# Optimization experiments

Measured on AMD Instinct MI355X. Metric: run time of the kernel, lower is better.

## Reference

```python
import jax, jax.numpy as jnp
import numpy as np

D_MODEL = 512
N_HEADS = 8
EDGE_FEAT_DIM = 4
NUM_GRAPHS = 64
NODES_PER_GRAPH = 128
N_NODES = NUM_GRAPHS * NODES_PER_GRAPH          # 8192
EDGES_PER_GRAPH = 4096                           # avg degree 32
N_EDGES = NUM_GRAPHS * EDGES_PER_GRAPH           # 262144


def setup_inputs() -> dict:
    key = jax.random.key(0)
    ks = jax.random.split(key, 12)
    s = 0.02
    x = jax.random.normal(ks[0], (N_NODES, D_MODEL), jnp.float32)
    # edges constrained within their graph (block-diagonal structure)
    g_of_e = jnp.arange(N_EDGES, dtype=jnp.int32) // EDGES_PER_GRAPH
    src = g_of_e * NODES_PER_GRAPH + jax.random.randint(ks[1], (N_EDGES,), 0, NODES_PER_GRAPH, jnp.int32)
    dst = g_of_e * NODES_PER_GRAPH + jax.random.randint(ks[2], (N_EDGES,), 0, NODES_PER_GRAPH, jnp.int32)
    edge_index = jnp.stack([src, dst]).astype(jnp.int32)
    edge_attr = jax.random.normal(ks[3], (N_EDGES, EDGE_FEAT_DIM), jnp.float32)
    batch = jnp.repeat(jnp.arange(NUM_GRAPHS, dtype=jnp.int32), NODES_PER_GRAPH)
    # projection weights (in,out) convention: y = x @ W + b
    Wq = jax.random.normal(ks[4], (D_MODEL, D_MODEL), jnp.float32) * s
    Wk = jax.random.normal(ks[5], (D_MODEL, D_MODEL), jnp.float32) * s
    Wv = jax.random.normal(ks[6], (D_MODEL, D_MODEL), jnp.float32) * s
    Wo = jax.random.normal(ks[7], (D_MODEL, D_MODEL), jnp.float32) * s
    bq = jnp.zeros((D_MODEL,), jnp.float32)
    bk = jnp.zeros((D_MODEL,), jnp.float32)
    bv = jnp.zeros((D_MODEL,), jnp.float32)
    bo = jnp.zeros((D_MODEL,), jnp.float32)
    # edge bias MLP: edge_feat_dim -> d_model -> n_heads
    W1 = jax.random.normal(ks[8], (EDGE_FEAT_DIM, D_MODEL), jnp.float32) * s
    b1 = jnp.zeros((D_MODEL,), jnp.float32)
    W2 = jax.random.normal(ks[9], (D_MODEL, N_HEADS), jnp.float32) * s
    b2 = jnp.zeros((N_HEADS,), jnp.float32)
    return {"x": x, "edge_index": edge_index, "edge_attr": edge_attr, "batch": batch,
            "n_g": NODES_PER_GRAPH,
            "Wq": Wq, "bq": bq, "Wk": Wk, "bk": bk, "Wv": Wv, "bv": bv,
            "Wo": Wo, "bo": bo, "W1": W1, "b1": b1, "W2": W2, "b2": b2}


def reference(x, edge_index, edge_attr, batch, n_g, Wq, bq, Wk, bk, Wv, bv, Wo, bo, W1, b1, W2, b2):
    # batch is contiguous equal-size blocks of n_g nodes per graph, so the
    # per-graph Python loop of the original collapses to a batched (G, n_g)
    # block-diagonal attention. Dropout is identity (eval / p used only in train).
    N, d_model = x.shape
    H = W2.shape[1]
    d_k = d_model // H
    G = N // n_g
    scale = 1.0 / float(np.sqrt(d_k))

    Q = (x @ Wq + bq).reshape(G, n_g, H, d_k)
    K = (x @ Wk + bk).reshape(G, n_g, H, d_k)
    V = (x @ Wv + bv).reshape(G, n_g, H, d_k)

    # (G, i, j, h) dense per-graph scores
    scores = jnp.einsum('gihd,gjhd->gijh', Q, K) * scale

    # edge bias: MLP(edge_attr) -> (E, H), scattered at (graph, local_src, local_dst)
    bias = jax.nn.relu(edge_attr @ W1 + b1) @ W2 + b2
    ge = edge_index[0] // n_g
    ls = edge_index[0] % n_g
    ld = edge_index[1] % n_g
    scores = scores.at[ge, ls, ld].add(bias)

    attn = jax.nn.softmax(scores, axis=2)  # softmax over j (keys), matches dim=1 of (i,j,h)
    out = jnp.einsum('gijh,gjhd->gihd', attn, V).reshape(N, d_model)
    return out @ Wo + bo
```

## Files before the change

kernel.cpp:

```cpp
#include <hip/hip_runtime.h>
#include <hip/hip_bf16.h>

#define E_TOTAL 262144
#define NG      128
#define GRAPHS  64
#define NHEADS  8
#define DKH     64
#define DMODEL  512
#define NNODES  8192

typedef __bf16 bf16x8 __attribute__((ext_vector_type(8)));
typedef float  f32x4  __attribute__((ext_vector_type(4)));
typedef short  s16x4  __attribute__((ext_vector_type(4)));
typedef unsigned short u16x8 __attribute__((ext_vector_type(8)));

typedef __attribute__((address_space(3))) char lds_char;
typedef const __attribute__((address_space(1))) char glb_char;

__device__ inline __hip_bfloat16 f2hbf(float f) { return __float2bfloat16(f); }
__device__ inline unsigned short f2u16(float f) {
    return __builtin_bit_cast(unsigned short, __float2bfloat16(f));
}
__device__ inline __bf16 f2bf(float f) {
    return __builtin_bit_cast(__bf16, f2u16(f));
}
__device__ inline bf16x8 cvt8(float4 lo, float4 hi) {
    bf16x8 o;
    o[0] = f2bf(lo.x); o[1] = f2bf(lo.y); o[2] = f2bf(lo.z); o[3] = f2bf(lo.w);
    o[4] = f2bf(hi.x); o[5] = f2bf(hi.y); o[6] = f2bf(hi.z); o[7] = f2bf(hi.w);
    return o;
}

__global__ __launch_bounds__(256) void prep_kernel(
    const float* __restrict__ Wq, const float* __restrict__ Wk,
    const float* __restrict__ Wv, const float* __restrict__ Wo,
    const float* __restrict__ W1, const float* __restrict__ b1,
    const float* __restrict__ W2, const float* __restrict__ b2,
    const float* __restrict__ x, __hip_bfloat16* __restrict__ xbf,
    __hip_bfloat16* __restrict__ wqkvt, __hip_bfloat16* __restrict__ wot,
    __hip_bfloat16* __restrict__ w1fragt, float* __restrict__ b1f,
    __hip_bfloat16* __restrict__ w2at, float* __restrict__ b2f)
{
    int blk = blockIdx.x, tid = threadIdx.x;
    if (blk < 256) {
        __shared__ __align__(16) __hip_bfloat16 tile[64][65];
        const float* src;
        __hip_bfloat16* dstT;
        int n0, k0, nb;
        if (blk < 192) {
            int nt = blk % 24, ktile = blk / 24;
            n0 = nt * 64; k0 = ktile * 64;
            if (n0 < 512)       { src = Wq; nb = n0; }
            else if (n0 < 1024) { src = Wk; nb = n0 - 512; }
            else                { src = Wv; nb = n0 - 1024; }
            dstT = wqkvt;
        } else {
            int t = blk - 192;
            n0 = (t % 8) * 64; k0 = (t / 8) * 64; nb = n0;
            src = Wo; dstT = wot;
        }
        #pragma unroll
        for (int i = 0; i < 16; ++i) {
            int idx = tid + i * 256;
            int kr = idx >> 6, nc = idx & 63;
            tile[kr][nc] = f2hbf(src[(size_t)(k0 + kr) * 512 + nb + nc]);
        }
        __syncthreads();
        #pragma unroll
        for (int i = 0; i < 16; ++i) {
            int idx = tid + i * 256;
            int nr = idx >> 6, kc = idx & 63;
            dstT[(size_t)(n0 + nr) * 512 + k0 + kc] = tile[kc][nr];
        }
    } else if (blk == 256) {
        __hip_bfloat16 z = f2hbf(0.f);
        for (int n = tid; n < 512; n += 256) {
            #pragma unroll
            for (int j = 0; j < 4; ++j) w1fragt[n * 4 + j] = f2hbf(W1[(size_t)j * 512 + n]);
        }
        for (int i = tid; i < 512; i += 256) b1f[i] = b1[i];
        for (int i = tid; i < 32 * 64 * 4; i += 256) {
            int t = i >> 8, lane = (i >> 2) & 63, j = i & 3;
            int q = lane >> 4, l = lane & 15;
            w2at[i] = (l < 8) ? f2hbf(W2[(size_t)(16 * t + 4 * q + j) * 8 + l]) : z;
        }
        if (tid < 8) b2f[tid] = b2[tid];
    } else {
        int base = (blk - 257) * 2048 + tid * 8;
        float4 lo = *(const float4*)(x + base);
        float4 hi = *(const float4*)(x + base + 4);
        *(bf16x8*)(xbf + base) = cvt8(lo, hi);
    }
}

__device__ __forceinline__ void gemm0_body(
    const __hip_bfloat16* __restrict__ A, const __hip_bfloat16* __restrict__ BT,
    int row0, int col0,
    const float* __restrict__ bq, const float* __restrict__ bk,
    const float* __restrict__ bv,
    __hip_bfloat16* __restrict__ qkv, __hip_bfloat16* __restrict__ vt,
    __hip_bfloat16* __restrict__ As, __hip_bfloat16* __restrict__ Bs)
{
    const int K = 512;
    int tid = threadIdx.x;
    int lane = tid & 63, quad = lane >> 4, l16 = lane & 15;
    int wave = tid >> 6, wi = wave >> 1, wj = wave & 1;

    f32x4 acc[4][4];
    #pragma unroll
    for (int a = 0; a < 4; a++)
        #pragma unroll
        for (int b = 0; b < 4; b++)
            #pragma unroll
            for (int r = 0; r < 4; r++) acc[a][b][r] = 0.f;

    const __hip_bfloat16* Ag0 = A + (size_t)(row0 + (tid >> 2)) * K + (tid & 3) * 8;
    const __hip_bfloat16* Ag1 = Ag0 + (size_t)64 * K;
    const __hip_bfloat16* Bg0 = BT + (size_t)(col0 + (tid >> 2)) * K + (tid & 3) * 8;
    const __hip_bfloat16* Bg1 = Bg0 + (size_t)64 * K;
    char* AsB = (char*)As;
    char* BsB = (char*)Bs;

#define G0STAGE(kt, buf) do { \
    __builtin_amdgcn_global_load_lds((glb_char*)(Ag0 + (kt) * 32), (lds_char*)(AsB + (buf) * 8192 + tid * 16), 16, 0, 0); \
    __builtin_amdgcn_global_load_lds((glb_char*)(Ag1 + (kt) * 32), (lds_char*)(AsB + (buf) * 8192 + 4096 + tid * 16), 16, 0, 0); \
    __builtin_amdgcn_global_load_lds((glb_char*)(Bg0 + (kt) * 32), (lds_char*)(BsB + (buf) * 8192 + tid * 16), 16, 0, 0); \
    __builtin_amdgcn_global_load_lds((glb_char*)(Bg1 + (kt) * 32), (lds_char*)(BsB + (buf) * 8192 + 4096 + tid * 16), 16, 0, 0); \
} while (0)

    G0STAGE(0, 0);
    G0STAGE(1, 1);

    #pragma unroll
    for (int kt = 0; kt < 16; ++kt) {
        if (kt < 15) asm volatile("s_waitcnt vmcnt(4)" ::: "memory");
        else         asm volatile("s_waitcnt vmcnt(0)" ::: "memory");
        __builtin_amdgcn_s_barrier();
        if (kt < 14) G0STAGE(kt + 2, (kt + 2) % 3);
        const __hip_bfloat16* Asc = As + (kt % 3) * 4096;
        const __hip_bfloat16* Bsc = Bs + (kt % 3) * 4096;
        bf16x8 af[4], bfr[4];
        #pragma unroll
        for (int t = 0; t < 4; t++)
            af[t] = *(const bf16x8*)&Asc[(wi * 64 + t * 16 + l16) * 32 + quad * 8];
        #pragma unroll
        for (int t = 0; t < 4; t++)
            bfr[t] = *(const bf16x8*)&Bsc[(wj * 64 + t * 16 + l16) * 32 + quad * 8];
        #pragma unroll
        for (int ti = 0; ti < 4; ti++)
            #pragma unroll
            for (int tj = 0; tj < 4; tj++)
                acc[ti][tj] = __builtin_amdgcn_mfma_f32_16x16x32_bf16(af[ti], bfr[tj], acc[ti][tj], 0, 0, 0);
    }
#undef G0STAGE

    #pragma unroll
    for (int ti = 0; ti < 4; ti++)
        #pragma unroll
        for (int tj = 0; tj < 4; tj++) {
            int c = col0 + wj * 64 + tj * 16 + l16;
            #pragma unroll
            for (int r = 0; r < 4; r++) {
                int rw = row0 + wi * 64 + ti * 16 + quad * 4 + r;
                float v = acc[ti][tj][r];
                if (c < 1024) {
                    v += (c < 512) ? bq[c] : bk[c - 512];
                    qkv[(size_t)rw * 1536 + c] = f2hbf(v);
                } else {
                    v += bv[c - 1024];
                    int g = rw >> 7, i = rw & 127, hh = (c - 1024) >> 6, d = (c - 1024) & 63;
                    vt[(((size_t)(g * 8 + hh)) * 64 + d) * 128 + i] = f2hbf(v);
                }
            }
        }
}

__device__ __forceinline__ void edge_body(
    int eblk,
    const float* __restrict__ ea,
    const __hip_bfloat16* __restrict__ w1fragt, const float* __restrict__ b1f,
    const __hip_bfloat16* __restrict__ w2at, const float* __restrict__ b2f,
    float* __restrict__ biasE)
{
    int tid = threadIdx.x, wave = tid >> 6, lane = tid & 63;
    int quad = lane >> 4, l16 = lane & 15;
    int eb = eblk * 256 + wave * 64;

    s16x4 eaf[4] = {};
    if (quad == 0) {
        #pragma unroll
        for (int gg = 0; gg < 4; ++gg) {
            float4 e4 = *(const float4*)(ea + (size_t)(eb + gg * 16 + l16) * 4);
            eaf[gg][0] = (short)f2u16(e4.x); eaf[gg][1] = (short)f2u16(e4.y);
            eaf[gg][2] = (short)f2u16(e4.z); eaf[gg][3] = (short)f2u16(e4.w);
        }
    }

    f32x4 c2[4];
    #pragma unroll
    for (int gg = 0; gg < 4; ++gg)
        #pragma unroll
        for (int r = 0; r < 4; ++r) c2[gg][r] = 0.f;

    #pragma unroll 4
    for (int t = 0; t < 32; ++t) {
        s16x4 a1 = *(const s16x4*)(w1fragt + ((size_t)t * 16 + l16) * 4);
        float4 b14 = *(const float4*)(b1f + t * 16 + quad * 4);
        s16x4 a2 = *(const s16x4*)(w2at + ((size_t)t * 64 + lane) * 4);
        #pragma unroll
        for (int gg = 0; gg < 4; ++gg) {
            f32x4 c1 = {0.f, 0.f, 0.f, 0.f};
            c1 = __builtin_amdgcn_mfma_f32_16x16x16bf16_1k(a1, eaf[gg], c1, 0, 0, 0);
            s16x4 hfrag;
            hfrag[0] = (short)f2u16(fmaxf(c1[0] + b14.x, 0.f));
            hfrag[1] = (short)f2u16(fmaxf(c1[1] + b14.y, 0.f));
            hfrag[2] = (short)f2u16(fmaxf(c1[2] + b14.z, 0.f));
            hfrag[3] = (short)f2u16(fmaxf(c1[3] + b14.w, 0.f));
            c2[gg] = __builtin_amdgcn_mfma_f32_16x16x16bf16_1k(a2, hfrag, c2[gg], 0, 0, 0);
        }
    }
    if (quad < 2) {
        #pragma unroll
        for (int gg = 0; gg < 4; ++gg) {
            #pragma unroll
            for (int r = 0; r < 4; ++r) {
                int hh = quad * 4 + r;
                biasE[(size_t)hh * E_TOTAL + eb + gg * 16 + l16] = c2[gg][r] + b2f[hh];
            }
        }
    }
}

__global__ __launch_bounds__(256) void mega_kernel(
    const __hip_bfloat16* __restrict__ A, const __hip_bfloat16* __restrict__ BT,
    const float* __restrict__ bq, const float* __restrict__ bk,
    const float* __restrict__ bv,
    __hip_bfloat16* __restrict__ qkv, __hip_bfloat16* __restrict__ vt,
    const float* __restrict__ ea,
    const __hip_bfloat16* __restrict__ w1fragt, const float* __restrict__ b1f,
    const __hip_bfloat16* __restrict__ w2at, const float* __restrict__ b2f,
    float* __restrict__ biasE)
{
    __shared__ __align__(16) __hip_bfloat16 As[3 * 128 * 32];
    __shared__ __align__(16) __hip_bfloat16 Bs[3 * 128 * 32];
    int blk = blockIdx.x;
    if (blk < 768) {
        gemm0_body(A, BT, (blk & 63) * 128, (blk >> 6) * 128,
                   bq, bk, bv, qkv, vt, As, Bs);
    } else {
        edge_body(blk - 768, ea, w1fragt, b1f, w2at, b2f, biasE);
    }
}

__global__ __launch_bounds__(256) void gemm1_kernel(
    const __hip_bfloat16* __restrict__ A, const __hip_bfloat16* __restrict__ BT,
    const float* __restrict__ bo, float* __restrict__ out)
{
    const int K = 512;
    __shared__ __align__(16) __hip_bfloat16 As[3 * 128 * 32];
    __shared__ __align__(16) __hip_bfloat16 Bs[3 * 64 * 32];
    int tid = threadIdx.x;
    int lane = tid & 63, quad = lane >> 4, l16 = lane & 15;
    int wave = tid >> 6, wi = wave >> 1, wj = wave & 1;
    int row0 = blockIdx.x * 128, col0 = blockIdx.y * 64;

    f32x4 acc[4][2];
    #pragma unroll
    for (int a = 0; a < 4; a++)
        #pragma unroll
        for (int b = 0; b < 2; b++)
            #pragma unroll
            for (int r = 0; r < 4; r++) acc[a][b][r] = 0.f;

    const __hip_bfloat16* Ag0 = A + (size_t)(row0 + (tid >> 2)) * K + (tid & 3) * 8;
    const __hip_bfloat16* Ag1 = Ag0 + (size_t)64 * K;
    const __hip_bfloat16* Bg  = BT + (size_t)(col0 + (tid >> 2)) * K + (tid & 3) * 8;
    char* AsB = (char*)As;
    char* BsB = (char*)Bs;

#define G1STAGE(kt, buf) do { \
    __builtin_amdgcn_global_load_lds((glb_char*)(Ag0 + (kt) * 32), (lds_char*)(AsB + (buf) * 8192 + tid * 16), 16, 0, 0); \
    __builtin_amdgcn_global_load_lds((glb_char*)(Ag1 + (kt) * 32), (lds_char*)(AsB + (buf) * 8192 + 4096 + tid * 16), 16, 0, 0); \
    __builtin_amdgcn_global_load_lds((glb_char*)(Bg + (kt) * 32),  (lds_char*)(BsB + (buf) * 4096 + tid * 16), 16, 0, 0); \
} while (0)

    G1STAGE(0, 0);
    G1STAGE(1, 1);

    #pragma unroll
    for (int kt = 0; kt < 16; ++kt) {
        if (kt < 15) asm volatile("s_waitcnt vmcnt(3)" ::: "memory");
        else         asm volatile("s_waitcnt vmcnt(0)" ::: "memory");
        __builtin_amdgcn_s_barrier();
        if (kt < 14) G1STAGE(kt + 2, (kt + 2) % 3);
        const __hip_bfloat16* Asc = As + (kt % 3) * 4096;
        const __hip_bfloat16* Bsc = Bs + (kt % 3) * 2048;
        bf16x8 af[4], bfr[2];
        #pragma unroll
        for (int t = 0; t < 4; t++)
            af[t] = *(const bf16x8*)&Asc[(wi * 64 + t * 16 + l16) * 32 + quad * 8];
        #pragma unroll
        for (int t = 0; t < 2; t++)
            bfr[t] = *(const bf16x8*)&Bsc[(wj * 32 + t * 16 + l16) * 32 + quad * 8];
        #pragma unroll
        for (int ti = 0; ti < 4; ti++)
            #pragma unroll
            for (int tj = 0; tj < 2; tj++)
                acc[ti][tj] = __builtin_amdgcn_mfma_f32_16x16x32_bf16(af[ti], bfr[tj], acc[ti][tj], 0, 0, 0);
    }
#undef G1STAGE

    #pragma unroll
    for (int ti = 0; ti < 4; ti++)
        #pragma unroll
        for (int tj = 0; tj < 2; tj++) {
            int c = col0 + wj * 32 + tj * 16 + l16;
            #pragma unroll
            for (int r = 0; r < 4; r++) {
                int rw = row0 + wi * 64 + ti * 16 + quad * 4 + r;
                out[(size_t)rw * 512 + c] = acc[ti][tj][r] + bo[c];
            }
        }
}

#define SS 132
__global__ __launch_bounds__(512) void attn_kernel(
    const __hip_bfloat16* __restrict__ qkv,
    const __hip_bfloat16* __restrict__ vt,
    const float* __restrict__ biasE,
    const int* __restrict__ eidx,
    __hip_bfloat16* __restrict__ O)
{
    __shared__ __align__(16) float S[128 * SS];
    int blk = blockIdx.x, g = blk & 63, h = blk >> 6;
    int tid = threadIdx.x, wave = tid >> 6, lane = tid & 63;
    int quad = lane >> 4, l16 = lane & 15;

    int   sa[8];
    float bvv[8];
    #pragma unroll
    for (int u = 0; u < 8; ++u) {
        int idx = g * 4096 + tid + u * 512;
        int ls = eidx[idx] & 127;
        int ld = eidx[E_TOTAL + idx] & 127;
        sa[u] = ls * SS + ld;
        bvv[u] = biasE[(size_t)h * E_TOTAL + idx];
    }

    const __hip_bfloat16* qbase = qkv + (size_t)(g * 128) * 1536 + h * 64;
    const __hip_bfloat16* kbase = qbase + 512;

    f32x4 acc[8];
    #pragma unroll
    for (int j = 0; j < 8; j++)
        #pragma unroll
        for (int r = 0; r < 4; r++) acc[j][r] = 0.f;

    #pragma unroll
    for (int k0 = 0; k0 < 64; k0 += 32) {
        int m = wave * 16 + l16;
        bf16x8 af = *(const bf16x8*)(qbase + (size_t)m * 1536 + k0 + quad * 8);
        #pragma unroll
        for (int tj = 0; tj < 8; tj++) {
            int n = tj * 16 + l16;
            bf16x8 bfr = *(const bf16x8*)(kbase + (size_t)n * 1536 + k0 + quad * 8);
            acc[tj] = __builtin_amdgcn_mfma_f32_16x16x32_bf16(af, bfr, acc[tj], 0, 0, 0);
        }
    }
    #pragma unroll
    for (int tj = 0; tj < 8; tj++)
        #pragma unroll
        for (int r = 0; r < 4; r++) {
            int i = wave * 16 + quad * 4 + r;
            int j = tj * 16 + l16;
            S[i * SS + j] = acc[tj][r] * 0.125f;
        }
    __syncthreads();

    #pragma unroll
    for (int u = 0; u < 8; ++u)
        atomicAdd(&S[sa[u]], bvv[u]);
    __syncthreads();

    #pragma unroll 4
    for (int r = wave * 16; r < wave * 16 + 16; ++r) {
        float2 v = *(const float2*)&S[r * SS + 2 * lane];
        float m = fmaxf(v.x, v.y);
        #pragma unroll
        for (int off = 32; off > 0; off >>= 1) m = fmaxf(m, __shfl_xor(m, off));
        float e0 = __expf(v.x - m), e1 = __expf(v.y - m);
        float s = e0 + e1;
        #pragma unroll
        for (int off = 32; off > 0; off >>= 1) s += __shfl_xor(s, off);
        float inv = 1.0f / s;
        float2 o; o.x = e0 * inv; o.y = e1 * inv;
        *(float2*)&S[r * SS + 2 * lane] = o;
    }
    __syncthreads();

    f32x4 oacc[4];
    #pragma unroll
    for (int j = 0; j < 4; j++)
        #pragma unroll
        for (int r = 0; r < 4; r++) oacc[j][r] = 0.f;

    const __hip_bfloat16* vbase = vt + (size_t)(g * 8 + h) * 64 * 128;
    #pragma unroll
    for (int k0 = 0; k0 < 128; k0 += 32) {
        int m = wave * 16 + l16;
        const float* p = &S[m * SS + k0 + quad * 8];
        f32x4 xa = *(const f32x4*)p;
        f32x4 xb = *(const f32x4*)(p + 4);
        bf16x8 af;
        af[0] = f2bf(xa[0]); af[1] = f2bf(xa[1]); af[2] = f2bf(xa[2]); af[3] = f2bf(xa[3]);
        af[4] = f2bf(xb[0]); af[5] = f2bf(xb[1]); af[6] = f2bf(xb[2]); af[7] = f2bf(xb[3]);
        #pragma unroll
        for (int tj = 0; tj < 4; tj++) {
            int d = tj * 16 + l16;
            bf16x8 bfr = *(const bf16x8*)(vbase + (size_t)d * 128 + k0 + quad * 8);
            oacc[tj] = __builtin_amdgcn_mfma_f32_16x16x32_bf16(af, bfr, oacc[tj], 0, 0, 0);
        }
    }
    #pragma unroll
    for (int tj = 0; tj < 4; tj++)
        #pragma unroll
        for (int r = 0; r < 4; r++) {
            int i = wave * 16 + quad * 4 + r;
            int d = tj * 16 + l16;
            O[(size_t)(g * 128 + i) * 512 + h * 64 + d] = f2hbf(oacc[tj][r]);
        }
}

#define WS_WQKVT 0x0
#define WS_WOT   0x180000
#define WS_W1FR  0x200000
#define WS_B1F   0x202000
#define WS_W2AT  0x202800
#define WS_B2F   0x206800
#define WS_QKV   0xA10000
#define WS_VT    0x2210000
#define WS_BIASE 0x2A10000
#define WS_O     0x3210000
#define WS_XBF   WS_O

extern "C" void kernel_launch(void* const* d_in, const int* in_sizes, int n_in,
                              void* d_out, int out_size, void* d_ws, size_t ws_size,
                              hipStream_t stream) {
    const float* x    = (const float*)d_in[0];
    const int*   eidx = (const int*)d_in[1];
    const float* ea   = (const float*)d_in[2];
    const float* Wq = (const float*)d_in[5];
    const float* bq = (const float*)d_in[6];
    const float* Wk = (const float*)d_in[7];
    const float* bk = (const float*)d_in[8];
    const float* Wv = (const float*)d_in[9];
    const float* bv = (const float*)d_in[10];
    const float* Wo = (const float*)d_in[11];
    const float* bo = (const float*)d_in[12];
    const float* W1 = (const float*)d_in[13];
    const float* b1 = (const float*)d_in[14];
    const float* W2 = (const float*)d_in[15];
    const float* b2 = (const float*)d_in[16];

    char* ws = (char*)d_ws;
    __hip_bfloat16* wqkvt   = (__hip_bfloat16*)(ws + WS_WQKVT);
    __hip_bfloat16* wot     = (__hip_bfloat16*)(ws + WS_WOT);
    __hip_bfloat16* w1fragt = (__hip_bfloat16*)(ws + WS_W1FR);
    float* b1f   = (float*)(ws + WS_B1F);
    __hip_bfloat16* w2at    = (__hip_bfloat16*)(ws + WS_W2AT);
    float* b2f   = (float*)(ws + WS_B2F);
    __hip_bfloat16* qkv = (__hip_bfloat16*)(ws + WS_QKV);
    __hip_bfloat16* vt  = (__hip_bfloat16*)(ws + WS_VT);
    float* biasE = (float*)(ws + WS_BIASE);
    __hip_bfloat16* O   = (__hip_bfloat16*)(ws + WS_O);
    __hip_bfloat16* xbf = (__hip_bfloat16*)(ws + WS_XBF);

    prep_kernel<<<257 + 2048, 256, 0, stream>>>(Wq, Wk, Wv, Wo, W1, b1, W2, b2,
                                                x, xbf,
                                                wqkvt, wot, w1fragt, b1f, w2at, b2f);
    mega_kernel<<<768 + E_TOTAL / 256, 256, 0, stream>>>(
        xbf, wqkvt, bq, bk, bv, qkv, vt,
        ea, w1fragt, b1f, w2at, b2f, biasE);
    attn_kernel<<<GRAPHS * NHEADS, 512, 0, stream>>>(qkv, vt, biasE, eidx, O);
    gemm1_kernel<<<dim3(NNODES / 128, 512 / 64), 256, 0, stream>>>(
        O, wot, bo, (float*)d_out);
}
```

Baseline: 211.6 us.

## Swap MFMA operands for vectorized epilogue stores and interleave GEMM/edge blocks

Swaps the A/B operands of MFMA calls in the QK GEMM, output GEMM and attention kernels so each lane holds four consecutive columns, which lets the epilogues write packed bf16x4/f32x4 stores instead of scalar ones. The V-path epilogue writes contiguous runs of the transposed V buffer. The mega kernel interleaves GEMM tiles and edge-MLP blocks (3 of every 7 blocks) to balance work across CUs. The attention kernel prefetches the first half of the V fragments before the softmax barrier to hide load latency, at the cost of extra registers.

```diff
diff --git a/kernel.cpp b/kernel.cpp
--- a/kernel.cpp
+++ b/kernel.cpp
@@ -10,9 +10,9 @@
 #define NNODES  8192
 
 typedef __bf16 bf16x8 __attribute__((ext_vector_type(8)));
+typedef __bf16 bf16x4 __attribute__((ext_vector_type(4)));
 typedef float  f32x4  __attribute__((ext_vector_type(4)));
 typedef short  s16x4  __attribute__((ext_vector_type(4)));
-typedef unsigned short u16x8 __attribute__((ext_vector_type(8)));
 
 typedef __attribute__((address_space(3))) char lds_char;
 typedef const __attribute__((address_space(1))) char glb_char;
@@ -93,6 +93,7 @@
     }
 }
 
+template <bool QKPATH>
 __device__ __forceinline__ void gemm0_body(
     const __hip_bfloat16* __restrict__ A, const __hip_bfloat16* __restrict__ BT,
     int row0, int col0,
@@ -149,30 +150,55 @@
         #pragma unroll
         for (int ti = 0; ti < 4; ti++)
             #pragma unroll
-            for (int tj = 0; tj < 4; tj++)
-                acc[ti][tj] = __builtin_amdgcn_mfma_f32_16x16x32_bf16(af[ti], bfr[tj], acc[ti][tj], 0, 0, 0);
+            for (int tj = 0; tj < 4; tj++) {
+                if constexpr (QKPATH)
+                    acc[ti][tj] = __builtin_amdgcn_mfma_f32_16x16x32_bf16(bfr[tj], af[ti], acc[ti][tj], 0, 0, 0);
+                else
+                    acc[ti][tj] = __builtin_amdgcn_mfma_f32_16x16x32_bf16(af[ti], bfr[tj], acc[ti][tj], 0, 0, 0);
+            }
     }
 #undef G0STAGE
 
-    #pragma unroll
-    for (int ti = 0; ti < 4; ti++)
+    if constexpr (QKPATH) {
+        int rbase = row0 + wi * 64 + l16;
+        int cb0 = col0 + wj * 64 + quad * 4;
+        const float* bias = (col0 < 512) ? bq : bk;
+        int boff = (col0 < 512) ? 0 : 512;
         #pragma unroll
         for (int tj = 0; tj < 4; tj++) {
-            int c = col0 + wj * 64 + tj * 16 + l16;
-            #pragma unroll
-            for (int r = 0; r < 4; r++) {
-                int rw = row0 + wi * 64 + ti * 16 + quad * 4 + r;
-                float v = acc[ti][tj][r];
-                if (c < 1024) {
-                    v += (c < 512) ? bq[c] : bk[c - 512];
-                    qkv[(size_t)rw * 1536 + c] = f2hbf(v);
-                } else {
-                    v += bv[c - 1024];
-                    int g = rw >> 7, i = rw & 127, hh = (c - 1024) >> 6, d = (c - 1024) & 63;
-                    vt[(((size_t)(g * 8 + hh)) * 64 + d) * 128 + i] = f2hbf(v);
-                }
+            int cb = cb0 + tj * 16;
+            float4 bb = *(const float4*)(bias + cb - boff);
+            #pragma unroll
+            for (int ti = 0; ti < 4; ti++) {
+                int row = rbase + ti * 16;
+                bf16x4 v;
+                v[0] = f2bf(acc[ti][tj][0] + bb.x);
+                v[1] = f2bf(acc[ti][tj][1] + bb.y);
+                v[2] = f2bf(acc[ti][tj][2] + bb.z);
+                v[3] = f2bf(acc[ti][tj][3] + bb.w);
+                *(bf16x4*)(qkv + (size_t)row * 1536 + cb) = v;
             }
         }
+    } else {
+        int g = row0 >> 7;
+        int i0 = wi * 64 + quad * 4;
+        #pragma unroll
+        for (int tj = 0; tj < 4; tj++) {
+            int c = col0 - 1024 + wj * 64 + tj * 16 + l16;
+            int hh = c >> 6, d = c & 63;
+            float bvv = bv[c];
+            __hip_bfloat16* vdst = vt + ((size_t)(g * 8 + hh) * 64 + d) * 128 + i0;
+            #pragma unroll
+            for (int ti = 0; ti < 4; ti++) {
+                bf16x4 v;
+                v[0] = f2bf(acc[ti][tj][0] + bvv);
+                v[1] = f2bf(acc[ti][tj][1] + bvv);
+                v[2] = f2bf(acc[ti][tj][2] + bvv);
+                v[3] = f2bf(acc[ti][tj][3] + bvv);
+                *(bf16x4*)(vdst + ti * 16) = v;
+            }
+        }
+    }
 }
 
 __device__ __forceinline__ void edge_body(
@@ -244,11 +270,16 @@
     __shared__ __align__(16) __hip_bfloat16 As[3 * 128 * 32];
     __shared__ __align__(16) __hip_bfloat16 Bs[3 * 128 * 32];
     int blk = blockIdx.x;
-    if (blk < 768) {
-        gemm0_body(A, BT, (blk & 63) * 128, (blk >> 6) * 128,
-                   bq, bk, bv, qkv, vt, As, Bs);
+    int u = blk / 7, v = blk % 7;
+    if (v < 3) {
+        int tile = u * 3 + v;
+        int row0 = (tile & 63) * 128, col0 = (tile >> 6) * 128;
+        if (col0 < 1024)
+            gemm0_body<true>(A, BT, row0, col0, bq, bk, bv, qkv, vt, As, Bs);
+        else
+            gemm0_body<false>(A, BT, row0, col0, bq, bk, bv, qkv, vt, As, Bs);
     } else {
-        edge_body(blk - 768, ea, w1fragt, b1f, w2at, b2f, biasE);
+        edge_body(u * 4 + (v - 3), ea, w1fragt, b1f, w2at, b2f, biasE);
     }
 }
 
@@ -306,21 +337,27 @@
         for (int ti = 0; ti < 4; ti++)
             #pragma unroll
             for (int tj = 0; tj < 2; tj++)
-                acc[ti][tj] = __builtin_amdgcn_mfma_f32_16x16x32_bf16(af[ti], bfr[tj], acc[ti][tj], 0, 0, 0);
+                acc[ti][tj] = __builtin_amdgcn_mfma_f32_16x16x32_bf16(bfr[tj], af[ti], acc[ti][tj], 0, 0, 0);
     }
 #undef G1STAGE
 
-    #pragma unroll
-    for (int ti = 0; ti < 4; ti++)
-        #pragma unroll
-        for (int tj = 0; tj < 2; tj++) {
-            int c = col0 + wj * 32 + tj * 16 + l16;
-            #pragma unroll
-            for (int r = 0; r < 4; r++) {
-                int rw = row0 + wi * 64 + ti * 16 + quad * 4 + r;
-                out[(size_t)rw * 512 + c] = acc[ti][tj][r] + bo[c];
-            }
-        }
+    int rbase = row0 + wi * 64 + l16;
+    int cb0 = col0 + wj * 32 + quad * 4;
+    #pragma unroll
+    for (int tj = 0; tj < 2; tj++) {
+        int cb = cb0 + tj * 16;
+        float4 bb = *(const float4*)(bo + cb);
+        #pragma unroll
+        for (int ti = 0; ti < 4; ti++) {
+            int row = rbase + ti * 16;
+            f32x4 v;
+            v[0] = acc[ti][tj][0] + bb.x;
+            v[1] = acc[ti][tj][1] + bb.y;
+            v[2] = acc[ti][tj][2] + bb.z;
+            v[3] = acc[ti][tj][3] + bb.w;
+            *(f32x4*)(out + (size_t)row * 512 + cb) = v;
+        }
+    }
 }
 
 #define SS 132
@@ -349,6 +386,7 @@
 
     const __hip_bfloat16* qbase = qkv + (size_t)(g * 128) * 1536 + h * 64;
     const __hip_bfloat16* kbase = qbase + 512;
+    const __hip_bfloat16* vbase = vt + (size_t)(g * 8 + h) * 64 * 128;
 
     f32x4 acc[8];
     #pragma unroll
@@ -364,17 +402,29 @@
         for (int tj = 0; tj < 8; tj++) {
             int n = tj * 16 + l16;
             bf16x8 bfr = *(const bf16x8*)(kbase + (size_t)n * 1536 + k0 + quad * 8);
-            acc[tj] = __builtin_amdgcn_mfma_f32_16x16x32_bf16(af, bfr, acc[tj], 0, 0, 0);
-        }
-    }
-    #pragma unroll
-    for (int tj = 0; tj < 8; tj++)
-        #pragma unroll
-        for (int r = 0; r < 4; r++) {
-            int i = wave * 16 + quad * 4 + r;
-            int j = tj * 16 + l16;
-            S[i * SS + j] = acc[tj][r] * 0.125f;
-        }
+            acc[tj] = __builtin_amdgcn_mfma_f32_16x16x32_bf16(bfr, af, acc[tj], 0, 0, 0);
+        }
+    }
+    {
+        int i = wave * 16 + l16;
+        #pragma unroll
+        for (int tj = 0; tj < 8; tj++) {
+            f32x4 sv;
+            sv[0] = acc[tj][0] * 0.125f;
+            sv[1] = acc[tj][1] * 0.125f;
+            sv[2] = acc[tj][2] * 0.125f;
+            sv[3] = acc[tj][3] * 0.125f;
+            *(f32x4*)&S[i * SS + tj * 16 + quad * 4] = sv;
+        }
+    }
+
+    bf16x8 vpre[8];
+    #pragma unroll
+    for (int kh = 0; kh < 2; kh++)
+        #pragma unroll
+        for (int tj = 0; tj < 4; tj++)
+            vpre[kh * 4 + tj] = *(const bf16x8*)(vbase + (size_t)(tj * 16 + l16) * 128 + kh * 32 + quad * 8);
+
     __syncthreads();
 
     #pragma unroll
@@ -404,7 +454,6 @@
         #pragma unroll
         for (int r = 0; r < 4; r++) oacc[j][r] = 0.f;
 
-    const __hip_bfloat16* vbase = vt + (size_t)(g * 8 + h) * 64 * 128;
     #pragma unroll
     for (int k0 = 0; k0 < 128; k0 += 32) {
         int m = wave * 16 + l16;
@@ -416,19 +465,25 @@
         af[4] = f2bf(xb[0]); af[5] = f2bf(xb[1]); af[6] = f2bf(xb[2]); af[7] = f2bf(xb[3]);
         #pragma unroll
         for (int tj = 0; tj < 4; tj++) {
-            int d = tj * 16 + l16;
-            bf16x8 bfr = *(const bf16x8*)(vbase + (size_t)d * 128 + k0 + quad * 8);
-            oacc[tj] = __builtin_amdgcn_mfma_f32_16x16x32_bf16(af, bfr, oacc[tj], 0, 0, 0);
-        }
-    }
-    #pragma unroll
-    for (int tj = 0; tj < 4; tj++)
-        #pragma unroll
-        for (int r = 0; r < 4; r++) {
-            int i = wave * 16 + quad * 4 + r;
-            int d = tj * 16 + l16;
-            O[(size_t)(g * 128 + i) * 512 + h * 64 + d] = f2hbf(oacc[tj][r]);
-        }
+            bf16x8 bfr = (k0 < 64)
+                ? vpre[(k0 >> 5) * 4 + tj]
+                : *(const bf16x8*)(vbase + (size_t)(tj * 16 + l16) * 128 + k0 + quad * 8);
+            oacc[tj] = __builtin_amdgcn_mfma_f32_16x16x32_bf16(bfr, af, oacc[tj], 0, 0, 0);
+        }
+    }
+    {
+        int i = wave * 16 + l16;
+        __hip_bfloat16* obase = O + (size_t)(g * 128 + i) * 512 + h * 64 + quad * 4;
+        #pragma unroll
+        for (int tj = 0; tj < 4; tj++) {
+            bf16x4 ov;
+            ov[0] = f2bf(oacc[tj][0]);
+            ov[1] = f2bf(oacc[tj][1]);
+            ov[2] = f2bf(oacc[tj][2]);
+            ov[3] = f2bf(oacc[tj][3]);
+            *(bf16x4*)(obase + tj * 16) = ov;
+        }
+    }
 }
 
 #define WS_WQKVT 0x0
@@ -478,7 +533,7 @@
     prep_kernel<<<257 + 2048, 256, 0, stream>>>(Wq, Wk, Wv, Wo, W1, b1, W2, b2,
                                                 x, xbf,
                                                 wqkvt, wot, w1fragt, b1f, w2at, b2f);
-    mega_kernel<<<768 + E_TOTAL / 256, 256, 0, stream>>>(
+    mega_kernel<<<1792, 256, 0, stream>>>(
         xbf, wqkvt, bq, bk, bv, qkv, vt,
         ea, w1fragt, b1f, w2at, b2f, biasE);
     attn_kernel<<<GRAPHS * NHEADS, 512, 0, stream>>>(qkv, vt, biasE, eidx, O);
```

Result: faster. 201.1 us (-5.0%).
